# Kernel tuning notes

Measured on AMD Instinct MI355X. Metric: run time of the kernel, lower is better.

## Reference

```python
import jax, jax.numpy as jnp
import numpy as np

WS = 7          # window size
NH = 6          # heads per block
H = 112
W = 112
SHIFTS = (0, 3, 0, 3)  # alternating W-MSA / SW-MSA over depths=[2,2]


def _ln(x, g, b, eps=1e-5):
    m = x.mean(-1, keepdims=True)
    v = x.var(-1, keepdims=True)
    return (x - m) / jnp.sqrt(v + eps) * g + b


def _rel_idx():
    coords = np.stack(np.meshgrid(np.arange(WS), np.arange(WS), indexing='ij'))
    flat = coords.reshape(2, -1)
    rel = (flat[:, :, None] - flat[:, None, :]).transpose(1, 2, 0)
    rel[:, :, 0] += WS - 1
    rel[:, :, 1] += WS - 1
    rel[:, :, 0] *= 2 * WS - 1
    return rel.sum(-1)  # (49, 49) indices into the (2*WS-1)^2 bias table


def _attn_mask(shift):
    # standard Swin shifted-window attention mask, (nW, 49, 49)
    img = np.zeros((H, W))
    cnt = 0
    for hs in (slice(0, -WS), slice(-WS, -shift), slice(-shift, None)):
        for ws_ in (slice(0, -WS), slice(-WS, -shift), slice(-shift, None)):
            img[hs, ws_] = cnt
            cnt += 1
    win = img.reshape(H // WS, WS, W // WS, WS).transpose(0, 2, 1, 3).reshape(-1, WS * WS)
    m = win[:, None, :] - win[:, :, None]
    return np.where(m != 0, -100.0, 0.0).astype(np.float32)


def _win_part(x):  # (B,H,W,C) -> (B*nW, 49, C)
    B, _, _, C = x.shape
    x = x.reshape(B, H // WS, WS, W // WS, WS, C).transpose(0, 1, 3, 2, 4, 5)
    return x.reshape(-1, WS * WS, C)


def _win_rev(w, B, C):  # (B*nW, 49, C) -> (B,H,W,C)
    x = w.reshape(B, H // WS, W // WS, WS, WS, C).transpose(0, 1, 3, 2, 4, 5)
    return x.reshape(B, H, W, C)


def setup_inputs() -> dict:
    key = jax.random.key(0)
    ks = jax.random.split(key, 8)
    C, NB, B = 180, 4, 2
    f = lambda k, s: jax.random.normal(k, s, dtype=jnp.float32) * 0.02
    return {
        'x': jax.random.normal(ks[0], (B, C, H, W), dtype=jnp.float32),
        'pe_g': jnp.ones((C,), jnp.float32), 'pe_b': jnp.zeros((C,), jnp.float32),
        'ln1_g': jnp.ones((NB, C), jnp.float32), 'ln1_b': jnp.zeros((NB, C), jnp.float32),
        'qkv_w': f(ks[1], (NB, C, 3 * C)), 'qkv_b': jnp.zeros((NB, 3 * C), jnp.float32),
        'proj_w': f(ks[2], (NB, C, C)), 'proj_b': jnp.zeros((NB, C), jnp.float32),
        'ln2_g': jnp.ones((NB, C), jnp.float32), 'ln2_b': jnp.zeros((NB, C), jnp.float32),
        'fc1_w': f(ks[3], (NB, C, 4 * C)), 'fc1_b': jnp.zeros((NB, 4 * C), jnp.float32),
        'fc2_w': f(ks[4], (NB, 4 * C, C)), 'fc2_b': jnp.zeros((NB, C), jnp.float32),
        'rpb': f(ks[5], (NB, (2 * WS - 1) ** 2, NH)),
        'fn_g': jnp.ones((C,), jnp.float32), 'fn_b': jnp.zeros((C,), jnp.float32),
    }


def reference(x, pe_g, pe_b, ln1_g, ln1_b, qkv_w, qkv_b, proj_w, proj_b,
              ln2_g, ln2_b, fc1_w, fc1_b, fc2_w, fc2_b, rpb, fn_g, fn_b):
    B, C = x.shape[0], x.shape[1]
    dh = C // NH
    scale = dh ** -0.5
    rel_idx = jnp.asarray(_rel_idx())
    mask3 = jnp.asarray(_attn_mask(3))
    nW = (H // WS) * (W // WS)

    t = x.reshape(B, C, H * W).transpose(0, 2, 1)  # (B, L, C) tokens
    t = _ln(t, pe_g, pe_b)                          # patch_norm
    for i, shift in enumerate(SHIFTS):
        h = _ln(t, ln1_g[i], ln1_b[i]).reshape(B, H, W, C)
        if shift:
            h = jnp.roll(h, (-shift, -shift), axis=(1, 2))
        w = _win_part(h)                                            # (B*nW, 49, C)
        qkv = (w @ qkv_w[i] + qkv_b[i]).reshape(-1, WS * WS, 3, NH, dh)
        qkv = qkv.transpose(2, 0, 3, 1, 4)                          # (3, B*nW, NH, 49, dh)
        q, k, v = qkv[0] * scale, qkv[1], qkv[2]
        attn = jnp.einsum('bhid,bhjd->bhij', q, k)
        bias = rpb[i][rel_idx].transpose(2, 0, 1)                   # (NH, 49, 49)
        attn = attn + bias[None]
        if shift:
            attn = attn.reshape(B, nW, NH, WS * WS, WS * WS) + mask3[None, :, None]
            attn = attn.reshape(-1, NH, WS * WS, WS * WS)
        attn = jax.nn.softmax(attn, axis=-1)
        o = jnp.einsum('bhij,bhjd->bhid', attn, v)
        o = o.transpose(0, 2, 1, 3).reshape(-1, WS * WS, C)
        o = o @ proj_w[i] + proj_b[i]
        h = _win_rev(o, B, C)
        if shift:
            h = jnp.roll(h, (shift, shift), axis=(1, 2))
        t = t + h.reshape(B, H * W, C)                              # residual (drop_path=id at eval)
        m = _ln(t, ln2_g[i], ln2_b[i])
        m = jax.nn.gelu(m @ fc1_w[i] + fc1_b[i], approximate=False)
        t = t + (m @ fc2_w[i] + fc2_b[i])
    t = _ln(t, fn_g, fn_b)
    return t.reshape(B, H, W, C).transpose(0, 3, 1, 2)  # SwinBlock permute back to BCHW
```

## Files before the change

kernel.cpp:

```cpp
#include <hip/hip_runtime.h>
#include <hip/hip_bf16.h>
#include <cmath>

typedef __hip_bfloat16 bf16;
typedef short short8 __attribute__((ext_vector_type(8)));
typedef float f32x4  __attribute__((ext_vector_type(4)));

#define Cc    180
#define KP1   192
#define KP2   736
#define Hh    112
#define Wwid  112
#define Ltok  12544
#define Bsz   2
#define TOK   25088
#define WSz   7
#define NHd   6
#define DHd   30
#define NWIN  256
#define P49   49

__device__ __forceinline__ float LD(const void* p, size_t i, int f) {
    if (f) return ((const float*)p)[i];
    return (float)((const bf16*)p)[i];
}
__device__ __forceinline__ void ST(void* p, size_t i, int f, float v) {
    if (f) ((float*)p)[i] = v;
    else   ((bf16*)p)[i] = (bf16)v;
}

__device__ __forceinline__ short bh(float x) { bf16 t = (bf16)x; return *(short*)&t; }
__device__ __forceinline__ short8 cvt8(float4 a, float4 b) {
    short8 o;
    o[0] = bh(a.x); o[1] = bh(a.y); o[2] = bh(a.z); o[3] = bh(a.w);
    o[4] = bh(b.x); o[5] = bh(b.y); o[6] = bh(b.z); o[7] = bh(b.w);
    return o;
}

__device__ __forceinline__ float wred(float v) {
    v += __shfl_xor(v, 1);
    v += __shfl_xor(v, 2);
    v += __shfl_xor(v, 4);
    v += __shfl_xor(v, 8);
    v += __shfl_xor(v, 16);
    v += __shfl_xor(v, 32);
    return v;
}

__global__ void k_detect(const unsigned short* __restrict__ xb, int* __restrict__ flag) {
    __shared__ int s;
    if (threadIdx.x == 0) s = 0;
    __syncthreads();
    int bad = 0;
    for (int i = threadIdx.x; i < 2048; i += 256) {
        int e = (xb[i] >> 7) & 0xFF;
        if (e >= 0xC8) bad = 1;
    }
    if (bad) atomicOr(&s, 1);
    __syncthreads();
    if (threadIdx.x == 0) flag[0] = s;
}

__global__ __launch_bounds__(256) void k_tr(const void* __restrict__ src, size_t woff,
                                            bf16* __restrict__ dst,
                                            int K, int N, int Kp, int Npad,
                                            const int* __restrict__ dflag) {
    int f = *dflag;
    int idx = blockIdx.x * 256 + threadIdx.x;
    if (idx >= Npad * Kp) return;
    int n = idx / Kp, k = idx % Kp;
    float v = (n < N && k < K) ? LD(src, woff + (size_t)k * N + n, f) : 0.f;
    dst[idx] = (bf16)v;
}

__global__ __launch_bounds__(256) void k_trq(const void* __restrict__ src, size_t woff,
                                             bf16* __restrict__ dst,
                                             const int* __restrict__ dflag) {
    int f = *dflag;
    int idx = blockIdx.x * 256 + threadIdx.x;
    if (idx >= 576 * KP1) return;
    int n = idx / KP1, k = idx % KP1;
    int sec = n / 192, rm = n % 192, hd = rm >> 5, d = rm & 31;
    float v = (d < 30 && k < 180) ? LD(src, woff + (size_t)k * 540 + sec * 180 + hd * 30 + d, f) : 0.f;
    dst[idx] = (bf16)v;
}

__global__ __launch_bounds__(256) void k_bias(const void* __restrict__ rpb,
                                              float* __restrict__ BT,
                                              const int* __restrict__ dflag) {
    int f = *dflag;
    int idx = blockIdx.x * 256 + threadIdx.x;
    if (idx >= 4 * NHd * 4096) return;
    int blk = idx / (NHd * 4096);
    int rem0 = idx % (NHd * 4096);
    int hd = rem0 >> 12, rem = rem0 & 4095;
    int i = rem >> 6, j = rem & 63;
    float v;
    if (i < 49 && j < 49) {
        int rel = (i / 7 - j / 7 + 6) * 13 + (i % 7 - j % 7 + 6);
        v = LD(rpb, (size_t)blk * 169 * NHd + (size_t)rel * NHd + hd, f);
    } else {
        v = -1.0e9f;
    }
    BT[idx] = v;
}

__global__ __launch_bounds__(256) void k_patchnorm(const void* __restrict__ x,
                                                   const void* __restrict__ g,
                                                   const void* __restrict__ b,
                                                   float* __restrict__ T,
                                                   const int* __restrict__ dflag) {
    int f = *dflag;
    int tokid = blockIdx.x * 4 + (threadIdx.x >> 6);
    int lane  = threadIdx.x & 63;
    int bb = tokid / Ltok, ll = tokid % Ltok;
    size_t base = (size_t)bb * Cc * Ltok + ll;
    float v0 = LD(x, base + (size_t)lane * Ltok, f);
    float v1 = LD(x, base + (size_t)(lane + 64) * Ltok, f);
    float v2 = (lane < 52) ? LD(x, base + (size_t)(lane + 128) * Ltok, f) : 0.f;
    float s  = wred(v0 + v1 + v2);
    float sq = wred(v0 * v0 + v1 * v1 + v2 * v2);
    float mean = s * (1.f / 180.f);
    float var  = sq * (1.f / 180.f) - mean * mean;
    float rstd = rsqrtf(var + 1e-5f);
    float* tp = T + (size_t)tokid * Cc;
    tp[lane]      = (v0 - mean) * rstd * LD(g, lane, f)      + LD(b, lane, f);
    tp[lane + 64] = (v1 - mean) * rstd * LD(g, lane + 64, f) + LD(b, lane + 64, f);
    if (lane < 52)
        tp[lane + 128] = (v2 - mean) * rstd * LD(g, lane + 128, f) + LD(b, lane + 128, f);
}

__global__ __launch_bounds__(256) void k_ln(const float* __restrict__ T,
                                            const void* __restrict__ g,
                                            const void* __restrict__ b,
                                            bf16* __restrict__ D,
                                            int windowed, int shift, int goff,
                                            const int* __restrict__ dflag) {
    int f = *dflag;
    int r    = blockIdx.x * 4 + (threadIdx.x >> 6);
    int lane = threadIdx.x & 63;
    int src;
    if (windowed) {
        int bb  = r / (NWIN * P49);
        int rem = r % (NWIN * P49);
        int wi = rem / P49, p = rem % P49;
        int wy = wi >> 4, wx = wi & 15;
        int py = p / 7, px = p % 7;
        int gh = (wy * 7 + py + shift) % Hh;
        int gw = (wx * 7 + px + shift) % Wwid;
        src = bb * Ltok + gh * Wwid + gw;
    } else {
        src = r;
    }
    const float* tp = T + (size_t)src * Cc;
    float v0 = tp[lane];
    float v1 = tp[lane + 64];
    float v2 = (lane < 52) ? tp[lane + 128] : 0.f;
    float s  = wred(v0 + v1 + v2);
    float sq = wred(v0 * v0 + v1 * v1 + v2 * v2);
    float mean = s * (1.f / 180.f);
    float var  = sq * (1.f / 180.f) - mean * mean;
    float rstd = rsqrtf(var + 1e-5f);
    bf16* dp = D + (size_t)r * KP1;
    dp[lane]      = (bf16)((v0 - mean) * rstd * LD(g, goff + lane, f)      + LD(b, goff + lane, f));
    dp[lane + 64] = (bf16)((v1 - mean) * rstd * LD(g, goff + lane + 64, f) + LD(b, goff + lane + 64, f));
    if (lane < 52)
        dp[lane + 128] = (bf16)((v2 - mean) * rstd * LD(g, goff + lane + 128, f) + LD(b, goff + lane + 128, f));
    else
        dp[lane + 128] = (bf16)0.f;
}

__global__ __launch_bounds__(256) void k_final(const float* __restrict__ T,
                                               const void* __restrict__ g,
                                               const void* __restrict__ b,
                                               void* __restrict__ out,
                                               const int* __restrict__ dflag) {
    int f = *dflag;
    int tokid = blockIdx.x * 4 + (threadIdx.x >> 6);
    int lane  = threadIdx.x & 63;
    int bb = tokid / Ltok, ll = tokid % Ltok;
    const float* tp = T + (size_t)tokid * Cc;
    float v0 = tp[lane];
    float v1 = tp[lane + 64];
    float v2 = (lane < 52) ? tp[lane + 128] : 0.f;
    float s  = wred(v0 + v1 + v2);
    float sq = wred(v0 * v0 + v1 * v1 + v2 * v2);
    float mean = s * (1.f / 180.f);
    float var  = sq * (1.f / 180.f) - mean * mean;
    float rstd = rsqrtf(var + 1e-5f);
    size_t base = (size_t)bb * Cc * Ltok + ll;
    ST(out, base + (size_t)lane * Ltok,        f, (v0 - mean) * rstd * LD(g, lane, f)      + LD(b, lane, f));
    ST(out, base + (size_t)(lane + 64) * Ltok, f, (v1 - mean) * rstd * LD(g, lane + 64, f) + LD(b, lane + 64, f));
    if (lane < 52)
        ST(out, base + (size_t)(lane + 128) * Ltok, f,
           (v2 - mean) * rstd * LD(g, lane + 128, f) + LD(b, lane + 128, f));
}

template <int EPI>
__global__ __launch_bounds__(256) void k_mgemm(const bf16* __restrict__ A,
                                               const bf16* __restrict__ Wt,
                                               const void* __restrict__ bias,
                                               size_t boff, int Nbias,
                                               bf16* __restrict__ OutB, int ldOut, int Nstore,
                                               float* __restrict__ OutF,
                                               int Kp, int shift, int rowoff,
                                               const int* __restrict__ dflag) {
    __shared__ __align__(16) char SM[64 * 72 * 4];
    short* Als = (short*)SM;
    short* Bls = (short*)(SM + 8192);
    float* Els = (float*)SM;
    int tid = threadIdx.x, lane = tid & 63, w = tid >> 6;
    int wr = w >> 1, wc = w & 1;
    int q = lane >> 4, c = lane & 15;
    int m0 = blockIdx.y * 128, n0 = blockIdx.x * 64;
    f32x4 acc[4][2] = {};

    int rowA0 = m0 + (tid >> 6) * 16 + (tid & 15);
    int rowW  = n0 + (tid >> 6) * 16 + (tid & 15);
    int koff  = ((tid >> 4) & 3) * 8;
    const bf16* pa0 = A + (size_t)rowA0 * Kp + koff;
    const bf16* pa1 = A + (size_t)(rowA0 + 64) * Kp + koff;
    const bf16* pw  = Wt + (size_t)rowW * Kp + koff;
    ulonglong2 rA0 = *(const ulonglong2*)pa0;
    ulonglong2 rA1 = *(const ulonglong2*)pa1;
    ulonglong2 rW  = *(const ulonglong2*)pw;

    for (int k0 = 0; k0 < Kp; k0 += 32) {
        *(ulonglong2*)&Als[tid * 8]         = rA0;
        *(ulonglong2*)&Als[(tid + 256) * 8] = rA1;
        *(ulonglong2*)&Bls[tid * 8]         = rW;
        __syncthreads();
        if (k0 + 32 < Kp) {
            rA0 = *(const ulonglong2*)(pa0 + k0 + 32);
            rA1 = *(const ulonglong2*)(pa1 + k0 + 32);
            rW  = *(const ulonglong2*)(pw  + k0 + 32);
        }
        short8 b0 = *(const short8*)&Bls[((wc * 2 + 0) * 64 + lane) * 8];
        short8 b1 = *(const short8*)&Bls[((wc * 2 + 1) * 64 + lane) * 8];
#pragma unroll
        for (int mt = 0; mt < 4; ++mt) {
            short8 a = *(const short8*)&Als[((wr * 4 + mt) * 64 + lane) * 8];
            acc[mt][0] = __builtin_amdgcn_mfma_f32_16x16x32_bf16(a, b0, acc[mt][0], 0, 0, 0);
            acc[mt][1] = __builtin_amdgcn_mfma_f32_16x16x32_bf16(a, b1, acc[mt][1], 0, 0, 0);
        }
        __syncthreads();
    }

    int f = *dflag;
#pragma unroll
    for (int Ph = 0; Ph < 2; ++Ph) {
        if (Ph) __syncthreads();
        if (wr == Ph) {
#pragma unroll
            for (int mt = 0; mt < 4; ++mt)
#pragma unroll
                for (int nt = 0; nt < 2; ++nt)
#pragma unroll
                    for (int r = 0; r < 4; ++r) {
                        int rl = mt * 16 + q * 4 + r;
                        int cl = (wc * 2 + nt) * 16 + c;
                        int col = n0 + cl;
                        float val = acc[mt][nt][r];
                        if (EPI == 4) {
                            int sec = col / 192, rm = col % 192;
                            int hd = rm >> 5, d = rm & 31;
                            if (d < 30) val += LD(bias, boff + sec * 180 + hd * 30 + d, f);
                            if (sec == 0) val *= 0.18257418583505536f;
                        } else if (EPI == 1) {
                            if (col < Nbias) val += LD(bias, boff + col, f);
                            val = 0.5f * val * (1.f + erff(val * 0.70710678118654752f));
                        } else {
                            if (col < Nstore) val += LD(bias, boff + col, f);
                        }
                        Els[rl * 72 + cl] = val;
                    }
        }
        __syncthreads();
        if (EPI == 1 || EPI == 4) {
#pragma unroll
            for (int it = 0; it < 2; ++it) {
                int ri = it * 256 + tid;
                int row = ri >> 3, c8 = ri & 7;
                int gcol = n0 + c8 * 8;
                if (gcol < Nstore) {
                    float4 v0 = *(float4*)&Els[row * 72 + c8 * 8];
                    float4 v1 = *(float4*)&Els[row * 72 + c8 * 8 + 4];
                    short8 o = cvt8(v0, v1);
                    *(ulonglong2*)(OutB + (size_t)(m0 + Ph * 64 + row) * ldOut + gcol) =
                        *(ulonglong2*)&o;
                }
            }
        } else {
#pragma unroll
            for (int it = 0; it < 4; ++it) {
                int ri = it * 256 + tid;
                int row = ri >> 4, c4 = ri & 15;
                int col = n0 + c4 * 4;
                if (col < Nstore) {
                    int grow = rowoff + m0 + Ph * 64 + row;
                    int tgt = grow;
                    if (EPI == 3) {
                        int bb  = grow / (NWIN * P49);
                        int rem = grow % (NWIN * P49);
                        int wi = rem / P49, p = rem % P49;
                        int wy = wi >> 4, wx = wi & 15;
                        int py = p / 7, px = p % 7;
                        int gh = (wy * 7 + py + shift) % Hh;
                        int gw = (wx * 7 + px + shift) % Wwid;
                        tgt = bb * Ltok + gh * Wwid + gw;
                    }
                    float4* tp = (float4*)(OutF + (size_t)tgt * Cc + col);
                    float4 t = *tp;
                    float4 e = *(float4*)&Els[row * 72 + c4 * 4];
                    t.x += e.x; t.y += e.y; t.z += e.z; t.w += e.w;
                    *tp = t;
                }
            }
        }
    }
}

__device__ __forceinline__ int regionOf(int g, int shift) {
    return (g < Hh - WSz) ? 0 : ((g < Hh - shift) ? 1 : 2);
}

__global__ __launch_bounds__(64) void k_mattn(const bf16* __restrict__ QKV,
                                              const bf16* __restrict__ Vt_unused,
                                              const float* __restrict__ BT,
                                              bf16* __restrict__ Ow,
                                              int shift, int w0) {
    __shared__ __align__(16) bf16 P[64 * 72];
    __shared__ __align__(16) bf16 Vl[32 * 72];
    int lane = threadIdx.x;
    int lw = blockIdx.x / NHd, hd = blockIdx.x % NHd;
    int r0 = lw * P49;
    int q = lane >> 4, c = lane & 15;

    const bf16* qb = QKV + (size_t)(r0 + c) * 576 + hd * 32 + q * 8;
    short8 qf[4], kf[4];
#pragma unroll
    for (int t = 0; t < 4; ++t) {
        qf[t] = *(const short8*)(qb + (size_t)t * 16 * 576);
        kf[t] = *(const short8*)(qb + 192 + (size_t)t * 16 * 576);
    }
    for (int t = lane; t < 32 * 15; t += 64) {
        int d = t / 15, p = 49 + t % 15;
        Vl[d * 72 + p] = (bf16)0.f;
    }
    for (int t = lane; t < P49 * 4; t += 64) {
        int p = t >> 2, ch = t & 3;
        ulonglong2 v = *(const ulonglong2*)(QKV + (size_t)(r0 + p) * 576 + 384 + hd * 32 + ch * 8);
        bf16* vv = (bf16*)&v;
#pragma unroll
        for (int j = 0; j < 8; ++j) Vl[(ch * 8 + j) * 72 + p] = vv[j];
    }

    f32x4 zero = {0.f, 0.f, 0.f, 0.f};
    f32x4 S[4][4];
#pragma unroll
    for (int mt = 0; mt < 4; ++mt)
#pragma unroll
        for (int nt = 0; nt < 4; ++nt)
            S[mt][nt] = __builtin_amdgcn_mfma_f32_16x16x32_bf16(qf[mt], kf[nt], zero, 0, 0, 0);

    const float* bt = BT + hd * 4096;
    int wi = (w0 + lw) & (NWIN - 1);
    int wy = wi >> 4, wx = wi & 15;
    int lj[4], li[4][4];
    if (shift) {
#pragma unroll
        for (int nt = 0; nt < 4; ++nt) {
            int j = nt * 16 + c;
            lj[nt] = (j < 49) ? regionOf(wy * 7 + j / 7, shift) * 3 + regionOf(wx * 7 + j % 7, shift) : -1;
        }
#pragma unroll
        for (int mt = 0; mt < 4; ++mt)
#pragma unroll
            for (int r = 0; r < 4; ++r) {
                int i = mt * 16 + q * 4 + r;
                li[mt][r] = (i < 49) ? regionOf(wy * 7 + i / 7, shift) * 3 + regionOf(wx * 7 + i % 7, shift) : -2;
            }
    }
    float rmax[4][4];
#pragma unroll
    for (int mt = 0; mt < 4; ++mt)
#pragma unroll
        for (int r = 0; r < 4; ++r) rmax[mt][r] = -3.0e38f;
#pragma unroll
    for (int mt = 0; mt < 4; ++mt)
#pragma unroll
        for (int nt = 0; nt < 4; ++nt)
#pragma unroll
            for (int r = 0; r < 4; ++r) {
                int i = mt * 16 + q * 4 + r, j = nt * 16 + c;
                float v = S[mt][nt][r] + bt[i * 64 + j];
                if (shift && li[mt][r] != lj[nt]) v -= 100.f;
                S[mt][nt][r] = v;
                rmax[mt][r] = fmaxf(rmax[mt][r], v);
            }
#pragma unroll
    for (int mt = 0; mt < 4; ++mt)
#pragma unroll
        for (int r = 0; r < 4; ++r) {
            float m = rmax[mt][r];
            m = fmaxf(m, __shfl_xor(m, 1));
            m = fmaxf(m, __shfl_xor(m, 2));
            m = fmaxf(m, __shfl_xor(m, 4));
            m = fmaxf(m, __shfl_xor(m, 8));
            rmax[mt][r] = m;
        }
    float rsum[4][4] = {};
#pragma unroll
    for (int mt = 0; mt < 4; ++mt)
#pragma unroll
        for (int nt = 0; nt < 4; ++nt)
#pragma unroll
            for (int r = 0; r < 4; ++r) {
                float e = __expf(S[mt][nt][r] - rmax[mt][r]);
                S[mt][nt][r] = e;
                rsum[mt][r] += e;
            }
#pragma unroll
    for (int mt = 0; mt < 4; ++mt)
#pragma unroll
        for (int r = 0; r < 4; ++r) {
            float s = rsum[mt][r];
            s += __shfl_xor(s, 1);
            s += __shfl_xor(s, 2);
            s += __shfl_xor(s, 4);
            s += __shfl_xor(s, 8);
            rsum[mt][r] = 1.f / s;
        }
#pragma unroll
    for (int mt = 0; mt < 4; ++mt)
#pragma unroll
        for (int nt = 0; nt < 4; ++nt)
#pragma unroll
            for (int r = 0; r < 4; ++r)
                P[(mt * 16 + q * 4 + r) * 72 + nt * 16 + c] = (bf16)(S[mt][nt][r] * rsum[mt][r]);
    __syncthreads();

    f32x4 O[4][2] = {};
#pragma unroll
    for (int ks = 0; ks < 2; ++ks) {
        short8 vf0 = *(const short8*)&Vl[(0  + c) * 72 + ks * 32 + q * 8];
        short8 vf1 = *(const short8*)&Vl[(16 + c) * 72 + ks * 32 + q * 8];
#pragma unroll
        for (int mt = 0; mt < 4; ++mt) {
            short8 pf = *(const short8*)&P[(mt * 16 + c) * 72 + ks * 32 + q * 8];
            O[mt][0] = __builtin_amdgcn_mfma_f32_16x16x32_bf16(pf, vf0, O[mt][0], 0, 0, 0);
            O[mt][1] = __builtin_amdgcn_mfma_f32_16x16x32_bf16(pf, vf1, O[mt][1], 0, 0, 0);
        }
    }
    int r0g = (w0 + lw) * P49;
#pragma unroll
    for (int mt = 0; mt < 4; ++mt)
#pragma unroll
        for (int nt = 0; nt < 2; ++nt)
#pragma unroll
            for (int r = 0; r < 4; ++r) {
                int i = mt * 16 + q * 4 + r, d = nt * 16 + c;
                if (i < 49 && d < 30)
                    Ow[(size_t)(r0g + i) * KP1 + hd * 30 + d] = (bf16)O[mt][nt][r];
            }
    if (hd == 0) {
        for (int idx = lane; idx < P49 * 12; idx += 64) {
            int p = idx / 12, cp = 180 + idx % 12;
            Ow[(size_t)(r0g + p) * KP1 + cp] = (bf16)0.f;
        }
    }
}

extern "C" void kernel_launch(void* const* d_in, const int* in_sizes, int n_in,
                              void* d_out, int out_size, void* d_ws, size_t ws_size,
                              hipStream_t stream) {
    const void* x      = d_in[0];
    const void* pe_g   = d_in[1];
    const void* pe_b   = d_in[2];
    const void* ln1_g  = d_in[3];
    const void* ln1_b  = d_in[4];
    const void* qkv_w  = d_in[5];
    const void* qkv_b  = d_in[6];
    const void* proj_w = d_in[7];
    const void* proj_b = d_in[8];
    const void* ln2_g  = d_in[9];
    const void* ln2_b  = d_in[10];
    const void* fc1_w  = d_in[11];
    const void* fc1_b  = d_in[12];
    const void* fc2_w  = d_in[13];
    const void* fc2_b  = d_in[14];
    const void* rpb    = d_in[15];
    const void* fn_g   = d_in[16];
    const void* fn_b   = d_in[17];

    const size_t wtQ = (size_t)576 * KP1, wtP = (size_t)192 * KP1;
    const size_t wtF1 = (size_t)768 * KP1, wtF2 = (size_t)192 * KP2;
    const size_t wtPerBlk = wtQ + wtP + wtF1 + wtF2;

    int*   dflag = (int*)d_ws;
    float* T     = (float*)((char*)d_ws + 256);
    bf16*  Abuf  = (bf16*)(T + (size_t)TOK * Cc);
    bf16*  Wts   = Abuf + (size_t)TOK * KP1;
    float* BT4   = (float*)(Wts + 4 * wtPerBlk);
    bf16*  Bbuf  = (bf16*)(BT4 + 4 * NHd * 4096);
    size_t fixed = (size_t)((char*)Bbuf - (char*)d_ws);

    int c = 1;
    while (c < 4 && fixed + (size_t)(TOK / c) * KP2 * 2 > ws_size) c <<= 1;
    int CM = TOK / c;
    int CW = (Bsz * NWIN) / c;

    dim3 b256(256);
    k_detect<<<1, b256, 0, stream>>>((const unsigned short*)x, dflag);

    for (int i = 0; i < 4; ++i) {
        bf16* wq  = Wts + i * wtPerBlk;
        bf16* wp  = wq + wtQ;
        bf16* wf1 = wp + wtP;
        bf16* wf2 = wf1 + wtF1;
        k_trq<<<(int)((wtQ + 255) / 256), b256, 0, stream>>>(qkv_w, (size_t)i * Cc * 540, wq, dflag);
        k_tr<<<(int)((wtP  + 255) / 256), b256, 0, stream>>>(proj_w, (size_t)i * Cc * Cc,  wp,  180, 180, KP1, 192, dflag);
        k_tr<<<(int)((wtF1 + 255) / 256), b256, 0, stream>>>(fc1_w,  (size_t)i * Cc * 720, wf1, 180, 720, KP1, 768, dflag);
        k_tr<<<(int)((wtF2 + 255) / 256), b256, 0, stream>>>(fc2_w,  (size_t)i * 720 * Cc, wf2, 720, 180, KP2, 192, dflag);
    }
    k_bias<<<(4 * NHd * 4096 + 255) / 256, b256, 0, stream>>>(rpb, BT4, dflag);

    k_patchnorm<<<TOK / 4, b256, 0, stream>>>(x, pe_g, pe_b, T, dflag);

    const int shifts[4] = {0, 3, 0, 3};
    for (int i = 0; i < 4; ++i) {
        int sh = shifts[i];
        bf16* wq  = Wts + i * wtPerBlk;
        bf16* wp  = wq + wtQ;
        bf16* wf1 = wp + wtP;
        bf16* wf2 = wf1 + wtF1;

        k_ln<<<TOK / 4, b256, 0, stream>>>(T, ln1_g, ln1_b, Abuf, 1, sh, i * Cc, dflag);
        for (int j = 0; j < c; ++j) {
            int R0 = j * CM;
            k_mgemm<4><<<dim3(9, CM / 128), b256, 0, stream>>>(
                Abuf + (size_t)R0 * KP1, wq, qkv_b, (size_t)i * 540, 540,
                Bbuf, 576, 576, nullptr, KP1, 0, 0, dflag);
            k_mattn<<<CW * NHd, 64, 0, stream>>>(Bbuf, nullptr, BT4 + i * NHd * 4096,
                                                 Abuf, sh, j * CW);
            k_mgemm<3><<<dim3(3, CM / 128), b256, 0, stream>>>(
                Abuf + (size_t)R0 * KP1, wp, proj_b, (size_t)i * Cc, Cc,
                nullptr, 0, Cc, T, KP1, sh, R0, dflag);
        }
        k_ln<<<TOK / 4, b256, 0, stream>>>(T, ln2_g, ln2_b, Abuf, 0, 0, i * Cc, dflag);
        for (int j = 0; j < c; ++j) {
            int R0 = j * CM;
            k_mgemm<1><<<dim3(12, CM / 128), b256, 0, stream>>>(
                Abuf + (size_t)R0 * KP1, wf1, fc1_b, (size_t)i * 720, 720,
                Bbuf, KP2, KP2, nullptr, KP1, 0, 0, dflag);
            k_mgemm<2><<<dim3(3, CM / 128), b256, 0, stream>>>(
                Bbuf, wf2, fc2_b, (size_t)i * Cc, Cc,
                nullptr, 0, Cc, T, KP2, 0, R0, dflag);
        }
    }

    k_final<<<TOK / 4, b256, 0, stream>>>(T, fn_g, fn_b, d_out, dflag);
}
```

Baseline: 941.5 us.

## Use wider 128x128 GEMM tiles for QKV and FC1 projections

Adds a new GEMM kernel with 128x128 output tiles, each wave holding a 4x4 block of MFMA accumulators. QKV and FC1 now use it, with the QKV weight padded to 640 rows so its N dimension divides into 128-wide tiles. The wider tile halves the number of blocks along N and raises reuse of each loaded A tile, cutting repeated activation reads. In exchange it uses more accumulator registers, can lower occupancy, and spends some MFMA work on padded columns.

```diff
diff --git a/kernel.cpp b/kernel.cpp
--- a/kernel.cpp
+++ b/kernel.cpp
@@ -78,10 +78,14 @@
                                              const int* __restrict__ dflag) {
     int f = *dflag;
     int idx = blockIdx.x * 256 + threadIdx.x;
-    if (idx >= 576 * KP1) return;
+    if (idx >= 640 * KP1) return;
     int n = idx / KP1, k = idx % KP1;
-    int sec = n / 192, rm = n % 192, hd = rm >> 5, d = rm & 31;
-    float v = (d < 30 && k < 180) ? LD(src, woff + (size_t)k * 540 + sec * 180 + hd * 30 + d, f) : 0.f;
+    float v = 0.f;
+    if (n < 576) {
+        int sec = n / 192, rm = n % 192, hd = rm >> 5, d = rm & 31;
+        if (d < 30 && k < 180)
+            v = LD(src, woff + (size_t)k * 540 + sec * 180 + hd * 30 + d, f);
+    }
     dst[idx] = (bf16)v;
 }
 
@@ -197,15 +201,114 @@
 }
 
 template <int EPI>
-__global__ __launch_bounds__(256) void k_mgemm(const bf16* __restrict__ A,
+__global__ __launch_bounds__(256) void k_wgemm(const bf16* __restrict__ A,
                                                const bf16* __restrict__ Wt,
                                                const void* __restrict__ bias,
                                                size_t boff, int Nbias,
                                                bf16* __restrict__ OutB, int ldOut, int Nstore,
+                                               const int* __restrict__ dflag) {
+    __shared__ __align__(16) char SM[64 * 68 * 4];
+    short* Als = (short*)SM;
+    short* Wls = (short*)(SM + 8192);
+    float* Els = (float*)SM;
+    int tid = threadIdx.x, lane = tid & 63, w = tid >> 6;
+    int wr = w >> 1, wc = w & 1;
+    int q = lane >> 4, c = lane & 15;
+    int m0 = blockIdx.y * 128, n0 = blockIdx.x * 128;
+    f32x4 acc[4][4] = {};
+
+    int rowS = (tid >> 6) * 16 + (tid & 15);
+    int koff = ((tid >> 4) & 3) * 8;
+    const bf16* pa0 = A + (size_t)(m0 + rowS) * KP1 + koff;
+    const bf16* pa1 = A + (size_t)(m0 + 64 + rowS) * KP1 + koff;
+    const bf16* pw0 = Wt + (size_t)(n0 + rowS) * KP1 + koff;
+    const bf16* pw1 = Wt + (size_t)(n0 + 64 + rowS) * KP1 + koff;
+    ulonglong2 rA0 = *(const ulonglong2*)pa0;
+    ulonglong2 rA1 = *(const ulonglong2*)pa1;
+    ulonglong2 rW0 = *(const ulonglong2*)pw0;
+    ulonglong2 rW1 = *(const ulonglong2*)pw1;
+
+    for (int k0 = 0; k0 < KP1; k0 += 32) {
+        *(ulonglong2*)&Als[tid * 8]         = rA0;
+        *(ulonglong2*)&Als[(tid + 256) * 8] = rA1;
+        *(ulonglong2*)&Wls[tid * 8]         = rW0;
+        *(ulonglong2*)&Wls[(tid + 256) * 8] = rW1;
+        __syncthreads();
+        if (k0 + 32 < KP1) {
+            rA0 = *(const ulonglong2*)(pa0 + k0 + 32);
+            rA1 = *(const ulonglong2*)(pa1 + k0 + 32);
+            rW0 = *(const ulonglong2*)(pw0 + k0 + 32);
+            rW1 = *(const ulonglong2*)(pw1 + k0 + 32);
+        }
+        short8 bfrag[4];
+#pragma unroll
+        for (int nt = 0; nt < 4; ++nt)
+            bfrag[nt] = *(const short8*)&Wls[((wc * 4 + nt) * 64 + lane) * 8];
+#pragma unroll
+        for (int mt = 0; mt < 4; ++mt) {
+            short8 a = *(const short8*)&Als[((wr * 4 + mt) * 64 + lane) * 8];
+#pragma unroll
+            for (int nt = 0; nt < 4; ++nt)
+                acc[mt][nt] = __builtin_amdgcn_mfma_f32_16x16x32_bf16(a, bfrag[nt], acc[mt][nt], 0, 0, 0);
+        }
+        __syncthreads();
+    }
+
+    int f = *dflag;
+#pragma unroll
+    for (int p = 0; p < 4; ++p) {
+        if (p) __syncthreads();
+        if (wr == (p >> 1) && wc == (p & 1)) {
+#pragma unroll
+            for (int mt = 0; mt < 4; ++mt)
+#pragma unroll
+                for (int nt = 0; nt < 4; ++nt)
+#pragma unroll
+                    for (int r = 0; r < 4; ++r) {
+                        int rl = mt * 16 + q * 4 + r;
+                        int cl = nt * 16 + c;
+                        int col = n0 + (p & 1) * 64 + cl;
+                        float val = acc[mt][nt][r];
+                        if (EPI == 4) {
+                            if (col < 576) {
+                                int sec = col / 192, rm = col % 192;
+                                int hd = rm >> 5, d = rm & 31;
+                                if (d < 30) val += LD(bias, boff + sec * 180 + hd * 30 + d, f);
+                                if (sec == 0) val *= 0.18257418583505536f;
+                            }
+                        } else {
+                            if (col < Nbias) val += LD(bias, boff + col, f);
+                            val = 0.5f * val * (1.f + erff(val * 0.70710678118654752f));
+                        }
+                        Els[rl * 68 + cl] = val;
+                    }
+        }
+        __syncthreads();
+#pragma unroll
+        for (int it = 0; it < 2; ++it) {
+            int ri = it * 256 + tid;
+            int row = ri >> 3, c8 = ri & 7;
+            int gcol = n0 + (p & 1) * 64 + c8 * 8;
+            if (gcol < Nstore) {
+                float4 v0 = *(float4*)&Els[row * 68 + c8 * 8];
+                float4 v1 = *(float4*)&Els[row * 68 + c8 * 8 + 4];
+                short8 o = cvt8(v0, v1);
+                *(ulonglong2*)(OutB + (size_t)(m0 + (p >> 1) * 64 + row) * ldOut + gcol) =
+                    *(ulonglong2*)&o;
+            }
+        }
+    }
+}
+
+template <int EPI>
+__global__ __launch_bounds__(256) void k_mgemm(const bf16* __restrict__ A,
+                                               const bf16* __restrict__ Wt,
+                                               const void* __restrict__ bias,
+                                               size_t boff, int Nstore,
                                                float* __restrict__ OutF,
                                                int Kp, int shift, int rowoff,
                                                const int* __restrict__ dflag) {
-    __shared__ __align__(16) char SM[64 * 72 * 4];
+    __shared__ __align__(16) char SM[64 * 68 * 4];
     short* Als = (short*)SM;
     short* Bls = (short*)(SM + 8192);
     float* Els = (float*)SM;
@@ -261,60 +364,34 @@
                         int cl = (wc * 2 + nt) * 16 + c;
                         int col = n0 + cl;
                         float val = acc[mt][nt][r];
-                        if (EPI == 4) {
-                            int sec = col / 192, rm = col % 192;
-                            int hd = rm >> 5, d = rm & 31;
-                            if (d < 30) val += LD(bias, boff + sec * 180 + hd * 30 + d, f);
-                            if (sec == 0) val *= 0.18257418583505536f;
-                        } else if (EPI == 1) {
-                            if (col < Nbias) val += LD(bias, boff + col, f);
-                            val = 0.5f * val * (1.f + erff(val * 0.70710678118654752f));
-                        } else {
-                            if (col < Nstore) val += LD(bias, boff + col, f);
-                        }
-                        Els[rl * 72 + cl] = val;
+                        if (col < Nstore) val += LD(bias, boff + col, f);
+                        Els[rl * 68 + cl] = val;
                     }
         }
         __syncthreads();
-        if (EPI == 1 || EPI == 4) {
-#pragma unroll
-            for (int it = 0; it < 2; ++it) {
-                int ri = it * 256 + tid;
-                int row = ri >> 3, c8 = ri & 7;
-                int gcol = n0 + c8 * 8;
-                if (gcol < Nstore) {
-                    float4 v0 = *(float4*)&Els[row * 72 + c8 * 8];
-                    float4 v1 = *(float4*)&Els[row * 72 + c8 * 8 + 4];
-                    short8 o = cvt8(v0, v1);
-                    *(ulonglong2*)(OutB + (size_t)(m0 + Ph * 64 + row) * ldOut + gcol) =
-                        *(ulonglong2*)&o;
+#pragma unroll
+        for (int it = 0; it < 4; ++it) {
+            int ri = it * 256 + tid;
+            int row = ri >> 4, c4 = ri & 15;
+            int col = n0 + c4 * 4;
+            if (col < Nstore) {
+                int grow = rowoff + m0 + Ph * 64 + row;
+                int tgt = grow;
+                if (EPI == 3) {
+                    int bb  = grow / (NWIN * P49);
+                    int rem = grow % (NWIN * P49);
+                    int wi = rem / P49, p = rem % P49;
+                    int wy = wi >> 4, wx = wi & 15;
+                    int py = p / 7, px = p % 7;
+                    int gh = (wy * 7 + py + shift) % Hh;
+                    int gw = (wx * 7 + px + shift) % Wwid;
+                    tgt = bb * Ltok + gh * Wwid + gw;
                 }
-            }
-        } else {
-#pragma unroll
-            for (int it = 0; it < 4; ++it) {
-                int ri = it * 256 + tid;
-                int row = ri >> 4, c4 = ri & 15;
-                int col = n0 + c4 * 4;
-                if (col < Nstore) {
-                    int grow = rowoff + m0 + Ph * 64 + row;
-                    int tgt = grow;
-                    if (EPI == 3) {
-                        int bb  = grow / (NWIN * P49);
-                        int rem = grow % (NWIN * P49);
-                        int wi = rem / P49, p = rem % P49;
-                        int wy = wi >> 4, wx = wi & 15;
-                        int py = p / 7, px = p % 7;
-                        int gh = (wy * 7 + py + shift) % Hh;
-                        int gw = (wx * 7 + px + shift) % Wwid;
-                        tgt = bb * Ltok + gh * Wwid + gw;
-                    }
-                    float4* tp = (float4*)(OutF + (size_t)tgt * Cc + col);
-                    float4 t = *tp;
-                    float4 e = *(float4*)&Els[row * 72 + c4 * 4];
-                    t.x += e.x; t.y += e.y; t.z += e.z; t.w += e.w;
-                    *tp = t;
-                }
+                float4* tp = (float4*)(OutF + (size_t)tgt * Cc + col);
+                float4 t = *tp;
+                float4 e = *(float4*)&Els[row * 68 + c4 * 4];
+                t.x += e.x; t.y += e.y; t.z += e.z; t.w += e.w;
+                *tp = t;
             }
         }
     }
@@ -325,7 +402,6 @@
 }
 
 __global__ __launch_bounds__(64) void k_mattn(const bf16* __restrict__ QKV,
-                                              const bf16* __restrict__ Vt_unused,
                                               const float* __restrict__ BT,
                                               bf16* __restrict__ Ow,
                                               int shift, int w0) {
@@ -493,7 +569,7 @@
     const void* fn_g   = d_in[16];
     const void* fn_b   = d_in[17];
 
-    const size_t wtQ = (size_t)576 * KP1, wtP = (size_t)192 * KP1;
+    const size_t wtQ = (size_t)640 * KP1, wtP = (size_t)192 * KP1;
     const size_t wtF1 = (size_t)768 * KP1, wtF2 = (size_t)192 * KP2;
     const size_t wtPerBlk = wtQ + wtP + wtF1 + wtF2;
 
@@ -538,24 +614,24 @@
         k_ln<<<TOK / 4, b256, 0, stream>>>(T, ln1_g, ln1_b, Abuf, 1, sh, i * Cc, dflag);
         for (int j = 0; j < c; ++j) {
             int R0 = j * CM;
-            k_mgemm<4><<<dim3(9, CM / 128), b256, 0, stream>>>(
+            k_wgemm<4><<<dim3(5, CM / 128), b256, 0, stream>>>(
                 Abuf + (size_t)R0 * KP1, wq, qkv_b, (size_t)i * 540, 540,
-                Bbuf, 576, 576, nullptr, KP1, 0, 0, dflag);
-            k_mattn<<<CW * NHd, 64, 0, stream>>>(Bbuf, nullptr, BT4 + i * NHd * 4096,
+                Bbuf, 576, 576, dflag);
+            k_mattn<<<CW * NHd, 64, 0, stream>>>(Bbuf, BT4 + i * NHd * 4096,
                                                  Abuf, sh, j * CW);
             k_mgemm<3><<<dim3(3, CM / 128), b256, 0, stream>>>(
                 Abuf + (size_t)R0 * KP1, wp, proj_b, (size_t)i * Cc, Cc,
-                nullptr, 0, Cc, T, KP1, sh, R0, dflag);
+                T, KP1, sh, R0, dflag);
         }
         k_ln<<<TOK / 4, b256, 0, stream>>>(T, ln2_g, ln2_b, Abuf, 0, 0, i * Cc, dflag);
         for (int j = 0; j < c; ++j) {
             int R0 = j * CM;
-            k_mgemm<1><<<dim3(12, CM / 128), b256, 0, stream>>>(
+            k_wgemm<1><<<dim3(6, CM / 128), b256, 0, stream>>>(
                 Abuf + (size_t)R0 * KP1, wf1, fc1_b, (size_t)i * 720, 720,
-                Bbuf, KP2, KP2, nullptr, KP1, 0, 0, dflag);
+                Bbuf, KP2, KP2, dflag);
             k_mgemm<2><<<dim3(3, CM / 128), b256, 0, stream>>>(
                 Bbuf, wf2, fc2_b, (size_t)i * Cc, Cc,
-                nullptr, 0, Cc, T, KP2, 0, R0, dflag);
+                T, KP2, 0, R0, dflag);
         }
     }
 
```

Result: slower. 1.401 ms (+48.8%).
